# Performance work log

Measured on AMD Instinct MI355X. Metric: run time of the kernel, lower is better.

Reference implementation:

```python
import jax, jax.numpy as jnp
import numpy as np

NT, NX = 64, 64
N_HALF = NT * NX // 2  # 2048 sites per checkerboard half

# mask[:, ::2] = False -> True at odd-x columns (the 'A' half)
_mask = np.ones((NT, NX), dtype=bool)
_mask[:, ::2] = False
IDX_A = jnp.asarray(np.where(_mask.reshape(-1))[0])   # [N_HALF]
IDX_B = jnp.asarray(np.where(~_mask.reshape(-1))[0])  # [N_HALF]


def setup_inputs() -> dict:
    key = jax.random.key(0)
    k0, k1, k2, k3, k4 = jax.random.split(key, 5)
    B = 4096
    scale = 1.0 / np.sqrt(N_HALF)
    return {
        "input_phi": jax.random.normal(k0, (B, NT, NX), dtype=jnp.float32),
        "W_s": jax.random.normal(k1, (N_HALF, N_HALF), dtype=jnp.float32) * scale,
        "b_s": jnp.zeros((N_HALF,), dtype=jnp.float32),
        "W_t": jax.random.normal(k2, (N_HALF, N_HALF), dtype=jnp.float32) * scale,
        "b_t": jnp.zeros((N_HALF,), dtype=jnp.float32),
    }


def _coupling(A, B, W_s, b_s, W_t, b_t):
    # Affine coupling: A' = A * exp(s(B)) + t(B); logDetJ = sum(s(B))
    s = jnp.tanh(B @ W_s.T + b_s)   # [batch, N_HALF]
    t = B @ W_t.T + b_t             # [batch, N_HALF]
    return A * jnp.exp(s) + t, jnp.sum(s, axis=-1)


def reference(input_phi, W_s, b_s, W_t, b_t):
    lead = input_phi.shape[:-2]
    phi = input_phi.reshape(*lead, NT * NX)
    A = phi[..., IDX_A]  # [batch, N_HALF]
    B = phi[..., IDX_B]
    A, logDetJc1 = _coupling(A, B, W_s, b_s, W_t, b_t)
    B, logDetJc2 = _coupling(B, A, W_s, b_s, W_t, b_t)
    out = jnp.zeros_like(phi).at[..., IDX_A].set(A).at[..., IDX_B].set(B)
    return out.reshape(*lead, NT, NX), logDetJc1 + logDetJc2
```

## Files before the change

### kernel.cpp

```cpp
#include <hip/hip_runtime.h>
#include <stdint.h>

#define BATCH 4096
#define NTX   4096
#define NH    2048
#define KDIM  2048

#define BM 128
#define BN 128
#define BK 32

typedef __bf16 bf16x8 __attribute__((ext_vector_type(8)));
typedef float  f32x4  __attribute__((ext_vector_type(4)));

__device__ __forceinline__ unsigned short f2bf(float f) {
    union { float f; unsigned u; } v; v.f = f;
    unsigned u = v.u;
    unsigned r = u + 0x7fffu + ((u >> 16) & 1u);
    return (unsigned short)(r >> 16);
}

__device__ __forceinline__ float fast_tanh(float x) {
    float e = __expf(x + x);
    return 1.f - 2.f / (e + 1.f);
}

typedef __attribute__((address_space(1))) void gvoid;
typedef __attribute__((address_space(3))) void lvoid;

__device__ __forceinline__ void async16(const unsigned short* g, unsigned short* l) {
    __builtin_amdgcn_global_load_lds((gvoid*)(void*)g, (lvoid*)l, 16, 0, 0);
}

__device__ __forceinline__ int lds_off(int R, int c) {
    return R * BK + (((c) + (R >> 1)) & 3) * 8;
}

__global__ void prep(const float* __restrict__ phi,
                     const float* __restrict__ Wsf,
                     const float* __restrict__ Wtf,
                     unsigned short* __restrict__ Bbf,
                     unsigned short* __restrict__ Wsb,
                     unsigned short* __restrict__ Wtb,
                     float* __restrict__ out)
{
    const int tid    = blockIdx.x * blockDim.x + threadIdx.x;
    const int stride = gridDim.x * blockDim.x;

    const float4* p4 = (const float4*)phi;
    for (int i = tid; i < (BATCH * NH / 4); i += stride) {
        float4 u = p4[2 * i], v = p4[2 * i + 1];
        uint2 o;
        o.x = (unsigned)f2bf(u.x) | ((unsigned)f2bf(u.z) << 16);
        o.y = (unsigned)f2bf(v.x) | ((unsigned)f2bf(v.z) << 16);
        ((uint2*)Bbf)[i] = o;
    }

    const float4* ws4 = (const float4*)Wsf;
    const float4* wt4 = (const float4*)Wtf;
    for (int i = tid; i < (NH * KDIM / 8); i += stride) {
        float4 u = ws4[2 * i], v = ws4[2 * i + 1];
        uint4 o;
        o.x = (unsigned)f2bf(u.x) | ((unsigned)f2bf(u.y) << 16);
        o.y = (unsigned)f2bf(u.z) | ((unsigned)f2bf(u.w) << 16);
        o.z = (unsigned)f2bf(v.x) | ((unsigned)f2bf(v.y) << 16);
        o.w = (unsigned)f2bf(v.z) | ((unsigned)f2bf(v.w) << 16);
        ((uint4*)Wsb)[i] = o;
        u = wt4[2 * i]; v = wt4[2 * i + 1];
        o.x = (unsigned)f2bf(u.x) | ((unsigned)f2bf(u.y) << 16);
        o.y = (unsigned)f2bf(u.z) | ((unsigned)f2bf(u.w) << 16);
        o.z = (unsigned)f2bf(v.x) | ((unsigned)f2bf(v.y) << 16);
        o.w = (unsigned)f2bf(v.z) | ((unsigned)f2bf(v.w) << 16);
        ((uint4*)Wtb)[i] = o;
    }

    for (int i = tid; i < BATCH; i += stride) out[(size_t)BATCH * NTX + i] = 0.f;
}

__global__ __launch_bounds__(256, 2) void coupling_gemm(
    const unsigned short* __restrict__ X,
    const unsigned short* __restrict__ Wsb,
    const unsigned short* __restrict__ Wtb,
    const float* __restrict__ bs,
    const float* __restrict__ bt,
    const float* __restrict__ phi,
    float* __restrict__ out,
    unsigned short* __restrict__ Xout,
    int parity)
{
    __shared__ unsigned short Xs[BM * BK];
    __shared__ unsigned short Ss[BN * BK];
    __shared__ unsigned short Ts[BN * BK];

    const int tid = threadIdx.x;
    const int m0 = blockIdx.x * BM;
    const int n0 = blockIdx.y * BN;

    f32x4 acc_s[4][4], acc_t[4][4];
    const f32x4 zf = {0.f, 0.f, 0.f, 0.f};
#pragma unroll
    for (int i = 0; i < 4; i++)
#pragma unroll
        for (int j = 0; j < 4; j++) { acc_s[i][j] = zf; acc_t[i][j] = zf; }

    const int rowA = tid >> 2;
    const int cgl  = (((tid & 3) - ((tid >> 3) & 3)) & 3) * 8;
    const unsigned short* Xg = X   + (size_t)(m0 + rowA) * KDIM + cgl;
    const unsigned short* Sg = Wsb + (size_t)(n0 + rowA) * KDIM + cgl;
    const unsigned short* Tg = Wtb + (size_t)(n0 + rowA) * KDIM + cgl;
    const size_t rstride = (size_t)64 * KDIM;
    unsigned short* Xl = Xs + tid * 8;
    unsigned short* Sl = Ss + tid * 8;
    unsigned short* Tl = Ts + tid * 8;

    const int wave = tid >> 6;
    const int lane = tid & 63;
    const int wm = (wave >> 1) * 64;
    const int wn = (wave & 1) * 64;
    const int lrow = lane & 15;
    const int kc   = lane >> 4;

    for (int k0 = 0; k0 < KDIM; k0 += BK) {
        __syncthreads();
        async16(Xg + k0,           Xl);
        async16(Xg + k0 + rstride, Xl + 2048);
        async16(Sg + k0,           Sl);
        async16(Sg + k0 + rstride, Sl + 2048);
        async16(Tg + k0,           Tl);
        async16(Tg + k0 + rstride, Tl + 2048);
        __syncthreads();

        bf16x8 a[4], vs[4], vt[4];
#pragma unroll
        for (int i = 0; i < 4; i++) {
            a[i]  = *(const bf16x8*)(Xs + lds_off(wm + i * 16 + lrow, kc));
            vs[i] = *(const bf16x8*)(Ss + lds_off(wn + i * 16 + lrow, kc));
            vt[i] = *(const bf16x8*)(Ts + lds_off(wn + i * 16 + lrow, kc));
        }
#pragma unroll
        for (int mi = 0; mi < 4; mi++)
#pragma unroll
            for (int ni = 0; ni < 4; ni++) {
                acc_s[mi][ni] = __builtin_amdgcn_mfma_f32_16x16x32_bf16(
                    a[mi], vs[ni], acc_s[mi][ni], 0, 0, 0);
                acc_t[mi][ni] = __builtin_amdgcn_mfma_f32_16x16x32_bf16(
                    a[mi], vt[ni], acc_t[mi][ni], 0, 0, 0);
            }
    }

    float* ldslot = out + (size_t)BATCH * NTX;
#pragma unroll
    for (int mi = 0; mi < 4; mi++) {
#pragma unroll
        for (int r = 0; r < 4; r++) {
            const int brow = m0 + wm + mi * 16 + (lane >> 4) * 4 + r;
            float ssum = 0.f;
#pragma unroll
            for (int ni = 0; ni < 4; ni++) {
                const int n = n0 + wn + ni * 16 + lrow;
                float s  = fast_tanh(acc_s[mi][ni][r] + bs[n]);
                float tv = acc_t[mi][ni][r] + bt[n];
                const size_t oidx = (size_t)brow * NTX + 2 * n + parity;
                float val = fmaf(phi[oidx], __expf(s), tv);
                out[oidx] = val;
                if (Xout) Xout[(size_t)brow * NH + n] = f2bf(val);
                ssum += s;
            }
            ssum += __shfl_xor(ssum, 1);
            ssum += __shfl_xor(ssum, 2);
            ssum += __shfl_xor(ssum, 4);
            ssum += __shfl_xor(ssum, 8);
            if (lrow == 0) atomicAdd(ldslot + brow, ssum);
        }
    }
}

extern "C" void kernel_launch(void* const* d_in, const int* in_sizes, int n_in,
                              void* d_out, int out_size, void* d_ws, size_t ws_size,
                              hipStream_t stream) {
    const float* phi = (const float*)d_in[0];
    const float* Wsf = (const float*)d_in[1];
    const float* bs  = (const float*)d_in[2];
    const float* Wtf = (const float*)d_in[3];
    const float* bt  = (const float*)d_in[4];
    float* out = (float*)d_out;

    char* ws = (char*)d_ws;
    unsigned short* Bbf  = (unsigned short*)(ws);
    unsigned short* Apbf = (unsigned short*)(ws + 16777216);
    unsigned short* Wsb  = (unsigned short*)(ws + 33554432);
    unsigned short* Wtb  = (unsigned short*)(ws + 41943040);

    prep<<<1024, 256, 0, stream>>>(phi, Wsf, Wtf, Bbf, Wsb, Wtb, out);

    coupling_gemm<<<dim3(32, 16), 256, 0, stream>>>(
        Bbf, Wsb, Wtb, bs, bt, phi, out, Apbf, 1);

    coupling_gemm<<<dim3(32, 16), 256, 0, stream>>>(
        Apbf, Wsb, Wtb, bs, bt, phi, out, nullptr, 0);
}
```

Before: 346.5 us.

## Double-buffer LDS tiles to overlap async global loads with MFMA compute

Replaces the single LDS tile set with two buffers. The next K-slice of X, Ws and Wt is prefetched with global_load_lds into one buffer while MFMAs consume the other, and each iteration now needs one barrier instead of two. The goal is to hide global-memory latency behind the matrix math. In exchange, LDS per block doubles to 48KB, which may limit occupancy. The last iteration also issues a wasted reload of slice zero.

Result: faster. 332.1 us (-4.2%).

```diff
diff --git a/kernel.cpp b/kernel.cpp
--- a/kernel.cpp
+++ b/kernel.cpp
@@ -9,6 +9,7 @@
 #define BM 128
 #define BN 128
 #define BK 32
+#define TILE_E (BM * BK)
 
 typedef __bf16 bf16x8 __attribute__((ext_vector_type(8)));
 typedef float  f32x4  __attribute__((ext_vector_type(4)));
@@ -88,9 +89,7 @@
     unsigned short* __restrict__ Xout,
     int parity)
 {
-    __shared__ unsigned short Xs[BM * BK];
-    __shared__ unsigned short Ss[BN * BK];
-    __shared__ unsigned short Ts[BN * BK];
+    __shared__ unsigned short lds[2][3][TILE_E];
 
     const int tid = threadIdx.x;
     const int m0 = blockIdx.x * BM;
@@ -109,9 +108,7 @@
     const unsigned short* Sg = Wsb + (size_t)(n0 + rowA) * KDIM + cgl;
     const unsigned short* Tg = Wtb + (size_t)(n0 + rowA) * KDIM + cgl;
     const size_t rstride = (size_t)64 * KDIM;
-    unsigned short* Xl = Xs + tid * 8;
-    unsigned short* Sl = Ss + tid * 8;
-    unsigned short* Tl = Ts + tid * 8;
+    const int lw = tid * 8;
 
     const int wave = tid >> 6;
     const int lane = tid & 63;
@@ -120,15 +117,39 @@
     const int lrow = lane & 15;
     const int kc   = lane >> 4;
 
-    for (int k0 = 0; k0 < KDIM; k0 += BK) {
-        __syncthreads();
-        async16(Xg + k0,           Xl);
-        async16(Xg + k0 + rstride, Xl + 2048);
-        async16(Sg + k0,           Sl);
-        async16(Sg + k0 + rstride, Sl + 2048);
-        async16(Tg + k0,           Tl);
-        async16(Tg + k0 + rstride, Tl + 2048);
-        __syncthreads();
+    {
+        unsigned short* b = &lds[0][0][0];
+        async16(Xg,           b + lw);
+        async16(Xg + rstride, b + lw + 2048);
+        b = &lds[0][1][0];
+        async16(Sg,           b + lw);
+        async16(Sg + rstride, b + lw + 2048);
+        b = &lds[0][2][0];
+        async16(Tg,           b + lw);
+        async16(Tg + rstride, b + lw + 2048);
+    }
+    __syncthreads();
+
+    const int NITER = KDIM / BK;
+    for (int k = 0; k < NITER; k++) {
+        const int cur = k & 1;
+        const int nxt = cur ^ 1;
+        {
+            const int k0n = (k + 1 < NITER) ? (k + 1) * BK : 0;
+            unsigned short* b = &lds[nxt][0][0];
+            async16(Xg + k0n,           b + lw);
+            async16(Xg + k0n + rstride, b + lw + 2048);
+            b = &lds[nxt][1][0];
+            async16(Sg + k0n,           b + lw);
+            async16(Sg + k0n + rstride, b + lw + 2048);
+            b = &lds[nxt][2][0];
+            async16(Tg + k0n,           b + lw);
+            async16(Tg + k0n + rstride, b + lw + 2048);
+        }
+
+        const unsigned short* Xs = &lds[cur][0][0];
+        const unsigned short* Ss = &lds[cur][1][0];
+        const unsigned short* Ts = &lds[cur][2][0];
 
         bf16x8 a[4], vs[4], vt[4];
 #pragma unroll
@@ -146,6 +167,8 @@
                 acc_t[mi][ni] = __builtin_amdgcn_mfma_f32_16x16x32_bf16(
                     a[mi], vt[ni], acc_t[mi][ni], 0, 0, 0);
             }
+
+        __syncthreads();
     }
 
     float* ldslot = out + (size_t)BATCH * NTX;
```

## Double-buffer LDS tiles to overlap async global loads with MFMA compute

Applied to the files above, without the earlier changes.

Splits shared memory into two ping-pong buffers so the async global-to-LDS loads for the next K slice are issued before the MFMAs on the current slice run. This removes one of the two barriers per iteration and is meant to hide global load latency behind compute. LDS use per block doubles to 48 KB, which may limit two-blocks-per-CU occupancy. The last iteration issues a redundant load of slice 0 into the idle buffer.

Result: faster. 333.0 us (-3.9%).

```diff
diff --git a/kernel.cpp b/kernel.cpp
--- a/kernel.cpp
+++ b/kernel.cpp
@@ -9,6 +9,7 @@
 #define BM 128
 #define BN 128
 #define BK 32
+#define TILE_E (BM * BK)
 
 typedef __bf16 bf16x8 __attribute__((ext_vector_type(8)));
 typedef float  f32x4  __attribute__((ext_vector_type(4)));
@@ -88,9 +89,8 @@
     unsigned short* __restrict__ Xout,
     int parity)
 {
-    __shared__ unsigned short Xs[BM * BK];
-    __shared__ unsigned short Ss[BN * BK];
-    __shared__ unsigned short Ts[BN * BK];
+    __shared__ unsigned short lds0[3][TILE_E];
+    __shared__ unsigned short lds1[3][TILE_E];
 
     const int tid = threadIdx.x;
     const int m0 = blockIdx.x * BM;
@@ -109,9 +109,7 @@
     const unsigned short* Sg = Wsb + (size_t)(n0 + rowA) * KDIM + cgl;
     const unsigned short* Tg = Wtb + (size_t)(n0 + rowA) * KDIM + cgl;
     const size_t rstride = (size_t)64 * KDIM;
-    unsigned short* Xl = Xs + tid * 8;
-    unsigned short* Sl = Ss + tid * 8;
-    unsigned short* Tl = Ts + tid * 8;
+    const int lw = tid * 8;
 
     const int wave = tid >> 6;
     const int lane = tid & 63;
@@ -120,22 +118,22 @@
     const int lrow = lane & 15;
     const int kc   = lane >> 4;
 
-    for (int k0 = 0; k0 < KDIM; k0 += BK) {
-        __syncthreads();
-        async16(Xg + k0,           Xl);
-        async16(Xg + k0 + rstride, Xl + 2048);
-        async16(Sg + k0,           Sl);
-        async16(Sg + k0 + rstride, Sl + 2048);
-        async16(Tg + k0,           Tl);
-        async16(Tg + k0 + rstride, Tl + 2048);
-        __syncthreads();
-
+    auto stage = [&](unsigned short (*buf)[TILE_E], int k0) {
+        async16(Xg + k0,           &buf[0][0] + lw);
+        async16(Xg + k0 + rstride, &buf[0][0] + lw + 2048);
+        async16(Sg + k0,           &buf[1][0] + lw);
+        async16(Sg + k0 + rstride, &buf[1][0] + lw + 2048);
+        async16(Tg + k0,           &buf[2][0] + lw);
+        async16(Tg + k0 + rstride, &buf[2][0] + lw + 2048);
+    };
+
+    auto compute = [&](const unsigned short (*buf)[TILE_E]) {
         bf16x8 a[4], vs[4], vt[4];
 #pragma unroll
         for (int i = 0; i < 4; i++) {
-            a[i]  = *(const bf16x8*)(Xs + lds_off(wm + i * 16 + lrow, kc));
-            vs[i] = *(const bf16x8*)(Ss + lds_off(wn + i * 16 + lrow, kc));
-            vt[i] = *(const bf16x8*)(Ts + lds_off(wn + i * 16 + lrow, kc));
+            a[i]  = *(const bf16x8*)(&buf[0][0] + lds_off(wm + i * 16 + lrow, kc));
+            vs[i] = *(const bf16x8*)(&buf[1][0] + lds_off(wn + i * 16 + lrow, kc));
+            vt[i] = *(const bf16x8*)(&buf[2][0] + lds_off(wn + i * 16 + lrow, kc));
         }
 #pragma unroll
         for (int mi = 0; mi < 4; mi++)
@@ -146,6 +144,19 @@
                 acc_t[mi][ni] = __builtin_amdgcn_mfma_f32_16x16x32_bf16(
                     a[mi], vt[ni], acc_t[mi][ni], 0, 0, 0);
             }
+    };
+
+    stage(lds0, 0);
+    __syncthreads();
+
+    const int NITER = KDIM / BK;
+    for (int kk = 0; kk < NITER; kk += 2) {
+        stage(lds1, (kk + 1) * BK);
+        compute(lds0);
+        __syncthreads();
+        stage(lds0, (kk + 2 < NITER) ? (kk + 2) * BK : 0);
+        compute(lds1);
+        __syncthreads();
     }
 
     float* ldslot = out + (size_t)BATCH * NTX;
```
